# Optimization experiments

Hardware: AMD Instinct MI355X
Metric: run time of the kernel (lower is better)

## Reference

```python
import jax, jax.numpy as jnp
import numpy as np

STRIDE = 1
PADDING = 1
GROUPS = 1


def setup_inputs() -> dict:
    key = jax.random.key(0)
    kx, kw, kb = jax.random.split(key, 3)
    x_int = jax.random.randint(kx, (16, 256, 56, 56), 0, 127, dtype=jnp.int32)
    weight_int = jax.random.randint(kw, (256, 256, 3, 3), 0, 127, dtype=jnp.int32)
    bias_int = jax.random.randint(kb, (256,), 0, 127, dtype=jnp.int32)
    return {"x_int": x_int, "weight_int": weight_int, "bias_int": bias_int}


def reference(x_int, weight_int, bias_int):
    # Integer conv2d with int32 accumulation, exactly F.conv2d semantics.
    y = jax.lax.conv_general_dilated(
        x_int,
        weight_int,
        window_strides=(STRIDE, STRIDE),
        padding=((PADDING, PADDING), (PADDING, PADDING)),
        dimension_numbers=("NCHW", "OIHW", "NCHW"),
        feature_group_count=GROUPS,
    )
    # bias broadcast over [B, Cout, H, W]
    return y + bias_int[None, :, None, None]
```

## Files before the change

kernel.cpp:

```cpp
#include <hip/hip_runtime.h>


typedef int v4i  __attribute__((ext_vector_type(4)));
typedef int v16i __attribute__((ext_vector_type(16)));

#define X8_ROWSTRIDE 1856
#define X8_IMGSTRIDE 107648
#define X8_BYTES     13778944
#define W8_CHUNK     18432
#define XS_OFF       55296
#define XS_BUF       30720

typedef const __attribute__((address_space(1))) unsigned char* gptr_t;
typedef __attribute__((address_space(3))) unsigned char* lptr_t;

__device__ __forceinline__ int pack4(const int* p, int stride) {
  return (p[0] & 255) | ((p[stride] & 255) << 8) |
         ((p[2 * stride] & 255) << 16) | ((p[3 * stride] & 255) << 24);
}

__global__ __launch_bounds__(256)
void pack_all(const int* __restrict__ x, const int* __restrict__ wgt,
              unsigned char* __restrict__ ws8) {
  const int blk = blockIdx.x;
  if (blk < 784) {
    const int gid = blk * 256 + threadIdx.x;
    const int srcg = gid & 1;
    int t = gid >> 1;
    const int sq = t % 14;  t /= 14;
    const int row = t % 56 + 1;
    const int cb  = t / 56;
    const int chunk = cb >> 4, b = cb & 15;
    const int ci0 = chunk * 32 + srcg * 16;
    const int* src = x + (b * 256 + ci0) * 3136 + (row - 1) * 56 + 4 * sq;
    v4i L[16];
    #pragma unroll
    for (int ch = 0; ch < 16; ++ch) L[ch] = *(const v4i*)(src + ch * 3136);
    unsigned char* dstrow = ws8 + cb * X8_IMGSTRIDE + row * X8_ROWSTRIDE;
    #pragma unroll
    for (int j = 0; j < 4; ++j) {
      const int slot = 4 * sq + 1 + j;
      v4i g;
      #pragma unroll
      for (int d = 0; d < 4; ++d)
        g[d] = (L[4 * d][j] & 255) | ((L[4 * d + 1][j] & 255) << 8) |
               ((L[4 * d + 2][j] & 255) << 16) | ((L[4 * d + 3][j] & 255) << 24);
      const int p = (srcg + (slot >> 2)) & 1;
      *(v4i*)(dstrow + slot * 32 + p * 16) = g;
    }
  } else if (blk < 1012) {
    const int g2 = (blk - 784) * 256 + threadIdx.x;
    const int cb = g2 / 456;
    const int r  = g2 - cb * 456;
    int off;
    if (r < 232) {
      const int row = r < 116 ? 0 : 57;
      const int rr = r % 116;
      off = row * X8_ROWSTRIDE + (rr >> 1) * 32 + (rr & 1) * 16;
    } else {
      const int r2 = r - 232;
      const int row = (r2 >> 2) + 1;
      const int slot = (r2 & 2) ? 57 : 0;
      off = row * X8_ROWSTRIDE + slot * 32 + (r2 & 1) * 16;
    }
    *(v4i*)(ws8 + cb * X8_IMGSTRIDE + off) = (v4i){0, 0, 0, 0};
  } else {
    const int gw = (blk - 1012) * 256 + threadIdx.x;
    const int p = gw & 1;
    int t = gw >> 1;
    const int tap = t % 9;  t /= 9;
    const int co = t & 63;
    const int tcc = t >> 6;
    const int chunk = tcc & 7, cotile = tcc >> 3;
    const int srcg = (p + (co >> 2)) & 1;
    const int ci0 = chunk * 32 + srcg * 16;
    const int* src = wgt + ((cotile * 64 + co) * 256 + ci0) * 9 + tap;
    v4i v = (v4i){pack4(src, 9), pack4(src + 36, 9),
                  pack4(src + 72, 9), pack4(src + 108, 9)};
    *(v4i*)(ws8 + X8_BYTES + (t * 9 + tap) * 32 + p * 16) = v;
  }
}

__device__ __forceinline__ void stage_chunk(const unsigned char* wg,
                                            const unsigned char* xg,
                                            unsigned char* ldsb, int c, int buf,
                                            int tid) {
  const unsigned char* wsrc = wg + c * W8_CHUNK;
  const unsigned char* xsrc = xg + c * (16 * X8_IMGSTRIDE);
  unsigned char* wdst = ldsb + buf * W8_CHUNK;
  unsigned char* xdst = ldsb + XS_OFF + buf * XS_BUF;
  #pragma unroll
  for (int i = 0; i < 2; ++i) {
    const int o = (tid + i * 512) * 16;
    __builtin_amdgcn_global_load_lds((gptr_t)(wsrc + o), (lptr_t)(wdst + o), 16, 0, 0);
  }
  if (tid < 128) {
    const int o = (1024 + tid) * 16;
    __builtin_amdgcn_global_load_lds((gptr_t)(wsrc + o), (lptr_t)(wdst + o), 16, 0, 0);
  } else {
    const int o = (tid - 128) * 16;
    __builtin_amdgcn_global_load_lds((gptr_t)(xsrc + o), (lptr_t)(xdst + o), 16, 0, 0);
  }
  #pragma unroll
  for (int i = 0; i < 3; ++i) {
    const int o = (384 + tid + i * 512) * 16;
    __builtin_amdgcn_global_load_lds((gptr_t)(xsrc + o), (lptr_t)(xdst + o), 16, 0, 0);
  }
}

#define LOADTAP(T, S)                                                     \
  do {                                                                    \
    const int kh_ = (T) / 3, kw_ = (T) % 3;                               \
    const unsigned char* xr_ = xs + rbase + kh_ * X8_ROWSTRIDE;           \
    fa0[S] = *(const v4i*)(wls + abase + (T) * 32);                       \
    fa1[S] = *(const v4i*)(wls + 9216 + abase + (T) * 32);                \
    fb[S][0] = *(const v4i*)(xr_ + boff[kw_][0]);                         \
    fb[S][1] = *(const v4i*)(xr_ + boff[kw_][1]);                         \
    fb[S][2] = *(const v4i*)(xr_ + boff[kw_][2]);                         \
    fb[S][3] = *(const v4i*)(xr_ + boff[kw_][3]);                         \
  } while (0)

__global__ __launch_bounds__(512, 2)
void conv_main(const unsigned char* __restrict__ ws8, const int* __restrict__ bias,
               int* __restrict__ out) {
  __shared__ __align__(16) unsigned char lds[3 * W8_CHUNK + 3 * XS_BUF];
  __shared__ int bls[64];

  const int tid = threadIdx.x, lane = tid & 63, wv = tid >> 6;
  const int n = lane & 31, gq = lane >> 5;
  const int tc = blockIdx.y;
  const int hb = blockIdx.x;
  const int hg = hb >> 4, b = hb & 15;
  const int h0 = hg * 14;

  if (tid < 64) {
    bls[tid] = bias[tc * 64 + tid];
    asm volatile("s_waitcnt lgkmcnt(0)" ::: "memory");
  }

  const int abase = n * 288 + (((gq + (n >> 2)) & 1) << 4);
  int boff[3][4];
  #pragma unroll
  for (int kw = 0; kw < 3; ++kw)
    #pragma unroll
    for (int bt = 0; bt < 4; ++bt) {
      int slot = bt * 16 + (n & 15) + kw;
      if (slot > 57) slot = 57;
      boff[kw][bt] = slot * 32 + (((gq + (slot >> 2)) & 1) << 4);
    }
  const int rbase = (2 * wv + (n >> 4)) * X8_ROWSTRIDE;

  v16i acc[2][4];
  #pragma unroll
  for (int i = 0; i < 2; ++i)
    #pragma unroll
    for (int j = 0; j < 4; ++j)
      acc[i][j] = (v16i){0,0,0,0,0,0,0,0,0,0,0,0,0,0,0,0};

  const unsigned char* wg = ws8 + X8_BYTES + tc * (8 * W8_CHUNK);
  const unsigned char* xg = ws8 + b * X8_IMGSTRIDE + h0 * X8_ROWSTRIDE;

  stage_chunk(wg, xg, lds, 0, 0, tid);
  stage_chunk(wg, xg, lds, 1, 1, tid);
  int buf = 0, nbuf = 2;
  for (int c = 0; c < 8; ++c) {
    if (c < 7) asm volatile("s_waitcnt vmcnt(6)" ::: "memory");
    else       asm volatile("s_waitcnt vmcnt(0)" ::: "memory");
    __builtin_amdgcn_s_barrier();
    asm volatile("" ::: "memory");
    if (c < 6) stage_chunk(wg, xg, lds, c + 2, nbuf, tid);
    if (wv < 7) {
      const unsigned char* wls = lds + buf * W8_CHUNK;
      const unsigned char* xs  = lds + XS_OFF + buf * XS_BUF;
      v4i fa0[2], fa1[2], fb[2][4];
      LOADTAP(0, 0);
      __builtin_amdgcn_sched_group_barrier(0x100, 6, 0);
      #pragma unroll
      for (int tap = 0; tap < 9; ++tap) {
        const int cur = tap & 1, nxt = cur ^ 1;
        if (tap < 8) LOADTAP(tap + 1, nxt);
        if (tap < 8)
          __builtin_amdgcn_sched_group_barrier(0x100, 6, 0);
        #pragma unroll
        for (int bt = 0; bt < 4; ++bt) {
          acc[0][bt] = __builtin_amdgcn_mfma_i32_32x32x32_i8(fa0[cur], fb[cur][bt], acc[0][bt], 0, 0, 0);
          acc[1][bt] = __builtin_amdgcn_mfma_i32_32x32x32_i8(fa1[cur], fb[cur][bt], acc[1][bt], 0, 0, 0);
        }
        __builtin_amdgcn_sched_group_barrier(0x008, 8, 0);
      }
    }
    buf  = (buf  == 2) ? 0 : buf  + 1;
    nbuf = (nbuf == 2) ? 0 : nbuf + 1;
  }

  if (wv >= 7) return;
  const int h = h0 + 2 * wv + (n >> 4);
  const int wbase = lane & 15;
  #pragma unroll
  for (int ct = 0; ct < 2; ++ct) {
    #pragma unroll
    for (int r = 0; r < 16; ++r) {
      const int co64 = ct * 32 + (r & 3) + 8 * (r >> 2) + 4 * gq;
      const int bv = bls[co64];
      int* orow = out + ((b * 256 + tc * 64 + co64) * 56 + h) * 56;
      #pragma unroll
      for (int bt = 0; bt < 4; ++bt) {
        const int w0 = bt * 16 + wbase;
        if (w0 < 56) orow[w0] = acc[ct][bt][r] + bv;
      }
    }
  }
}

extern "C" void kernel_launch(void* const* d_in, const int* in_sizes, int n_in,
                              void* d_out, int out_size, void* d_ws, size_t ws_size,
                              hipStream_t stream) {
  const int* x    = (const int*)d_in[0];
  const int* w    = (const int*)d_in[1];
  const int* bias = (const int*)d_in[2];
  unsigned char* ws8 = (unsigned char*)d_ws;
  hipLaunchKernelGGL(pack_all, dim3(1156), dim3(256), 0, stream, x, w, ws8);
  hipLaunchKernelGGL(conv_main, dim3(64, 4, 1), dim3(512), 0, stream,
                     ws8, bias, (int*)d_out);
}
```

Baseline: 131.0 us.

## Shrink conv tiles to 8 rows with 256-thread blocks and double buffering

Result: no change. 130.2 us (-0.7%).

```diff
diff --git a/kernel.cpp b/kernel.cpp
--- a/kernel.cpp
+++ b/kernel.cpp
@@ -8,11 +8,16 @@
 #define X8_IMGSTRIDE 107648
 #define X8_BYTES     13778944
 #define W8_CHUNK     18432
-#define XS_OFF       55296
-#define XS_BUF       30720
+#define WBUF         18432
+#define XBUF         20480
+#define LBUF         38912
 
 typedef const __attribute__((address_space(1))) unsigned char* gptr_t;
 typedef __attribute__((address_space(3))) unsigned char* lptr_t;
+
+__device__ __forceinline__ void gll(const unsigned char* g, unsigned char* l) {
+  __builtin_amdgcn_global_load_lds((gptr_t)g, (lptr_t)l, 16, 0, 0);
+}
 
 __device__ __forceinline__ int pack4(const int* p, int stride) {
   return (p[0] & 255) | ((p[stride] & 255) << 8) |
@@ -87,24 +92,28 @@
                                             int tid) {
   const unsigned char* wsrc = wg + c * W8_CHUNK;
   const unsigned char* xsrc = xg + c * (16 * X8_IMGSTRIDE);
-  unsigned char* wdst = ldsb + buf * W8_CHUNK;
-  unsigned char* xdst = ldsb + XS_OFF + buf * XS_BUF;
-  #pragma unroll
-  for (int i = 0; i < 2; ++i) {
-    const int o = (tid + i * 512) * 16;
-    __builtin_amdgcn_global_load_lds((gptr_t)(wsrc + o), (lptr_t)(wdst + o), 16, 0, 0);
+  unsigned char* wdst = ldsb + buf * LBUF;
+  unsigned char* xdst = wdst + WBUF;
+  #pragma unroll
+  for (int i = 0; i < 4; ++i) {
+    const int o = (tid + i * 256) * 16;
+    gll(wsrc + o, wdst + o);
   }
   if (tid < 128) {
     const int o = (1024 + tid) * 16;
-    __builtin_amdgcn_global_load_lds((gptr_t)(wsrc + o), (lptr_t)(wdst + o), 16, 0, 0);
+    gll(wsrc + o, wdst + o);
   } else {
     const int o = (tid - 128) * 16;
-    __builtin_amdgcn_global_load_lds((gptr_t)(xsrc + o), (lptr_t)(xdst + o), 16, 0, 0);
-  }
-  #pragma unroll
-  for (int i = 0; i < 3; ++i) {
-    const int o = (384 + tid + i * 512) * 16;
-    __builtin_amdgcn_global_load_lds((gptr_t)(xsrc + o), (lptr_t)(xdst + o), 16, 0, 0);
+    gll(xsrc + o, xdst + o);
+  }
+  #pragma unroll
+  for (int i = 5; i < 9; ++i) {
+    const int o = (tid + i * 256 - 1152) * 16;
+    gll(xsrc + o, xdst + o);
+  }
+  if (tid < 128) {
+    const int o = (1152 + tid) * 16;
+    gll(xsrc + o, xdst + o);
   }
 }
 
@@ -120,10 +129,10 @@
     fb[S][3] = *(const v4i*)(xr_ + boff[kw_][3]);                         \
   } while (0)
 
-__global__ __launch_bounds__(512, 2)
+__global__ __launch_bounds__(256, 2)
 void conv_main(const unsigned char* __restrict__ ws8, const int* __restrict__ bias,
                int* __restrict__ out) {
-  __shared__ __align__(16) unsigned char lds[3 * W8_CHUNK + 3 * XS_BUF];
+  __shared__ __align__(16) unsigned char lds[2 * LBUF];
   __shared__ int bls[64];
 
   const int tid = threadIdx.x, lane = tid & 63, wv = tid >> 6;
@@ -131,7 +140,7 @@
   const int tc = blockIdx.y;
   const int hb = blockIdx.x;
   const int hg = hb >> 4, b = hb & 15;
-  const int h0 = hg * 14;
+  const int h0 = hg * 8;
 
   if (tid < 64) {
     bls[tid] = bias[tc * 64 + tid];
@@ -161,17 +170,16 @@
   const unsigned char* xg = ws8 + b * X8_IMGSTRIDE + h0 * X8_ROWSTRIDE;
 
   stage_chunk(wg, xg, lds, 0, 0, tid);
-  stage_chunk(wg, xg, lds, 1, 1, tid);
-  int buf = 0, nbuf = 2;
+  int buf = 0;
+  #pragma unroll 1
   for (int c = 0; c < 8; ++c) {
-    if (c < 7) asm volatile("s_waitcnt vmcnt(6)" ::: "memory");
-    else       asm volatile("s_waitcnt vmcnt(0)" ::: "memory");
+    asm volatile("s_waitcnt vmcnt(0)" ::: "memory");
     __builtin_amdgcn_s_barrier();
     asm volatile("" ::: "memory");
-    if (c < 6) stage_chunk(wg, xg, lds, c + 2, nbuf, tid);
-    if (wv < 7) {
-      const unsigned char* wls = lds + buf * W8_CHUNK;
-      const unsigned char* xs  = lds + XS_OFF + buf * XS_BUF;
+    if (c < 7) stage_chunk(wg, xg, lds, c + 1, buf ^ 1, tid);
+    {
+      const unsigned char* wls = lds + buf * LBUF;
+      const unsigned char* xs  = wls + WBUF;
       v4i fa0[2], fa1[2], fb[2][4];
       LOADTAP(0, 0);
       __builtin_amdgcn_sched_group_barrier(0x100, 6, 0);
@@ -189,11 +197,9 @@
         __builtin_amdgcn_sched_group_barrier(0x008, 8, 0);
       }
     }
-    buf  = (buf  == 2) ? 0 : buf  + 1;
-    nbuf = (nbuf == 2) ? 0 : nbuf + 1;
-  }
-
-  if (wv >= 7) return;
+    buf ^= 1;
+  }
+
   const int h = h0 + 2 * wv + (n >> 4);
   const int wbase = lane & 15;
   #pragma unroll
@@ -220,6 +226,6 @@
   const int* bias = (const int*)d_in[2];
   unsigned char* ws8 = (unsigned char*)d_ws;
   hipLaunchKernelGGL(pack_all, dim3(1156), dim3(256), 0, stream, x, w, ws8);
-  hipLaunchKernelGGL(conv_main, dim3(64, 4, 1), dim3(512), 0, stream,
+  hipLaunchKernelGGL(conv_main, dim3(112, 4, 1), dim3(256), 0, stream,
                      ws8, bias, (int*)d_out);
 }
```
